# Optimization experiments

Measured on AMD Instinct MI355X. Metric: run time of the kernel, lower is better.

## Reference

```python
import jax, jax.numpy as jnp
import numpy as np

DIM, N_HEAD, N_KV, HEAD_DIM = 2048, 16, 4, 128
ROPE_BASE = 10000.0
ROPE_FACTOR = 1.0  # YaRN with factor=1 == plain RoPE


def setup_inputs() -> dict:
    key = jax.random.key(0)
    k1, k2, k3, k4 = jax.random.split(key, 4)
    b, s = 4, 2048
    sc = 1.0 / np.sqrt(DIM)
    return {
        "x": jax.random.normal(k1, (b, s, DIM), dtype=jnp.float32),
        "Wq": jax.random.normal(k2, (DIM, DIM), dtype=jnp.float32) * sc,
        "Wkv": jax.random.normal(k3, (2 * N_KV * HEAD_DIM, DIM), dtype=jnp.float32) * sc,
        "Wo": jax.random.normal(k4, (DIM, DIM), dtype=jnp.float32) * sc,
    }


def _rope_cos_sin(seqlen, start_pos=0):
    inv_freq = 1.0 / (ROPE_BASE ** (jnp.arange(0, HEAD_DIM, 2, dtype=jnp.float32) / HEAD_DIM))
    pos = (jnp.arange(seqlen, dtype=jnp.float32) + start_pos) / ROPE_FACTOR
    ang = pos[:, None] * inv_freq  # (s, hd/2)
    cos = jnp.concatenate([jnp.cos(ang), jnp.cos(ang)], axis=-1)  # (s, hd)
    sin = jnp.concatenate([jnp.sin(ang), jnp.sin(ang)], axis=-1)
    return cos[None, :, None, :], sin[None, :, None, :]  # (1, s, 1, hd)


def _rotate_half(t):
    h = HEAD_DIM // 2
    return jnp.concatenate([-t[..., h:], t[..., :h]], axis=-1)


def reference(x, Wq, Wkv, Wo):
    b, s, dim = x.shape
    G = N_HEAD // N_KV  # query heads per kv head
    q = (x @ Wq.T).reshape(b, s, N_HEAD, HEAD_DIM)                 # (b,s,H,hd)
    kv = (x @ Wkv.T).reshape(b, s, 2, N_KV, HEAD_DIM)
    k, v = kv[:, :, 0], kv[:, :, 1]                                # (b,s,KV,hd)
    cos, sin = _rope_cos_sin(s)
    q = q * cos + _rotate_half(q) * sin
    k = k * cos + _rotate_half(k) * sin
    # grouped attention: head h attends kv head h // G (matches repeat_interleave)
    qg = q.transpose(0, 2, 1, 3).reshape(b, N_KV, G, s, HEAD_DIM)  # (b,KV,G,s,hd)
    kt = k.transpose(0, 2, 1, 3)                                   # (b,KV,s,hd)
    vt = v.transpose(0, 2, 1, 3)
    scale = 1.0 / jnp.sqrt(jnp.asarray(HEAD_DIM, dtype=x.dtype))
    scores = jnp.einsum('bkgqd,bkpd->bkgqp', qg, kt) * scale       # (b,KV,G,s,s)
    causal = jnp.tril(jnp.ones((s, s), dtype=bool))
    scores = jnp.where(causal, scores, jnp.asarray(-jnp.inf, dtype=scores.dtype))
    probs = jax.nn.softmax(scores, axis=-1)
    out = jnp.einsum('bkgqp,bkpd->bkgqd', probs, vt)               # (b,KV,G,s,hd)
    out = out.reshape(b, N_HEAD, s, HEAD_DIM).transpose(0, 2, 1, 3).reshape(b, s, dim)
    return out @ Wo.T
```

## Files before the change

### kernel.cpp

```cpp
#include <hip/hip_runtime.h>
#include <hip/hip_bf16.h>

typedef __hip_bfloat16 bf16;
typedef __attribute__((ext_vector_type(4))) float f32x4;
typedef __attribute__((ext_vector_type(16))) float f32x16;
typedef __attribute__((ext_vector_type(8))) short short8;
typedef __attribute__((ext_vector_type(4))) unsigned u32x4;

#define NHEAD 16
#define NKV 4
#define HD 128
#define BATCH 4
#define SEQ 2048
#define DIMM 2048
#define NROWS (BATCH*SEQ)
#define QKVN (DIMM + 2*NKV*HD)

__device__ inline void gload_lds16(const bf16* g, bf16* l) {
  __builtin_amdgcn_global_load_lds(
      (const __attribute__((address_space(1))) unsigned int*)g,
      (__attribute__((address_space(3))) unsigned int*)l, 16, 0, 0);
}

__device__ inline unsigned cvtpk(float a, float b) {
  unsigned r;
  asm("v_cvt_pk_bf16_f32 %0, %1, %2" : "=v"(r) : "v"(a), "v"(b));
  return r;
}
__device__ inline void pswap(unsigned& x, unsigned& y) {
  asm volatile("v_permlane32_swap_b32 %0, %1" : "+v"(x), "+v"(y));
}
__device__ inline float bf2f(short s) {
  return __uint_as_float(((unsigned)(unsigned short)s) << 16);
}
__device__ inline short f2bfbits(float f) {
  bf16 h = __float2bfloat16(f);
  return *reinterpret_cast<short*>(&h);
}

#define CVTN0 ((size_t)NROWS * DIMM)
#define CVTN1 ((size_t)DIMM * DIMM)
#define CVTN2 ((size_t)2 * NKV * HD * DIMM)
#define CVTN3 ((size_t)DIMM * DIMM)
__global__ void cvt_all(const float* __restrict__ x, const float* __restrict__ wq,
                        const float* __restrict__ wkv, const float* __restrict__ wo,
                        bf16* __restrict__ xb, bf16* __restrict__ wqb,
                        bf16* __restrict__ wkvb, bf16* __restrict__ wob) {
  const size_t total = CVTN0 + CVTN1 + CVTN2 + CVTN3;
  for (size_t i = ((size_t)blockIdx.x * blockDim.x + threadIdx.x) * 4; i < total;
       i += (size_t)gridDim.x * blockDim.x * 4) {
    const float* s;
    bf16* d;
    size_t off;
    if (i < CVTN0) { s = x; d = xb; off = i; }
    else if (i < CVTN0 + CVTN1) { s = wq; d = wqb; off = i - CVTN0; }
    else if (i < CVTN0 + CVTN1 + CVTN2) { s = wkv; d = wkvb; off = i - CVTN0 - CVTN1; }
    else { s = wo; d = wob; off = i - CVTN0 - CVTN1 - CVTN2; }
    const float4 v = *reinterpret_cast<const float4*>(s + off);
    alignas(8) bf16 t[4] = {__float2bfloat16(v.x), __float2bfloat16(v.y),
                            __float2bfloat16(v.z), __float2bfloat16(v.w)};
    *reinterpret_cast<uint2*>(d + off) = *reinterpret_cast<const uint2*>(t);
  }
}

__device__ inline void store_c(float* p, float v) { *p = v; }
__device__ inline void store_c(bf16* p, float v) { *p = __float2bfloat16(v); }

template <typename OutT>
__global__ __launch_bounds__(512, 2) void gemm256(
    const bf16* __restrict__ A, const bf16* __restrict__ B0,
    const bf16* __restrict__ B1, OutT* __restrict__ C,
    int N, int K, int Nsplit, int MI8) {
  __shared__ __align__(16) short As[2][2][256 * 32];
  __shared__ __align__(16) short Bs[2][2][256 * 32];
  const int tid = threadIdx.x;
  const int w = tid >> 6, l = tid & 63;
  const int bid = blockIdx.x;
  const int xcd = bid & 7, q = bid >> 3;
  const int mi = q % MI8, j = q / MI8;
  const int m0 = (xcd * MI8 + mi) * 256, n0 = j * 256;
  const bf16* Ap = A + (size_t)m0 * K;
  const bf16* Bp = (n0 < Nsplit) ? (B0 + (size_t)n0 * K)
                                 : (B1 + (size_t)(n0 - Nsplit) * K);
  const int wr = w >> 2, wc = w & 3;
  const int lr = l & 15, lc = l >> 4;
  const int swz = lc ^ (((lr >> 3) & 1) << 1);

  f32x4 acc[8][4] = {};
  const int KT = K >> 6;

  auto stage = [&](int kt, int kh, int buf) {
#pragma unroll
    for (int jj = 0; jj < 2; ++jj) {
      const int cbase = jj * 512 + w * 64;
      const int ch = cbase + l;
      const int row = ch >> 2, c = ch & 3;
      const int sc = c ^ (((row >> 3) & 1) << 1);
      const int gcol = kt * 64 + kh * 32 + sc * 8;
      gload_lds16(Ap + (size_t)row * K + gcol, (bf16*)&As[buf][kh][cbase * 8]);
      gload_lds16(Bp + (size_t)row * K + gcol, (bf16*)&Bs[buf][kh][cbase * 8]);
    }
  };

  stage(0, 0, 0);
  stage(0, 1, 0);
  stage(1, 0, 1);

  for (int kt = 0; kt < KT; ++kt) {
    const int cur = kt & 1;
#pragma unroll
    for (int kh = 0; kh < 2; ++kh) {
      if (kt < KT - 1) {
        asm volatile("s_waitcnt vmcnt(8)" ::: "memory");
      } else if (kh == 0) {
        asm volatile("s_waitcnt vmcnt(4)" ::: "memory");
      } else {
        asm volatile("s_waitcnt vmcnt(0)" ::: "memory");
      }
      __builtin_amdgcn_s_barrier();
      __builtin_amdgcn_sched_barrier(0);

      short8 a[8], b[4];
      const short* Ab = &As[cur][kh][0];
      const short* Bb = &Bs[cur][kh][0];
#pragma unroll
      for (int mr = 0; mr < 8; ++mr)
        a[mr] = *(const short8*)&Ab[(wr * 128 + mr * 16 + lr) * 32 + swz * 8];
#pragma unroll
      for (int nr = 0; nr < 4; ++nr)
        b[nr] = *(const short8*)&Bb[(wc * 64 + nr * 16 + lr) * 32 + swz * 8];

      {
        const int g = 2 * kt + kh + 3;
        const int st = g >> 1;
        if (st < KT) stage(st, g & 1, st & 1);
      }

      __builtin_amdgcn_s_setprio(1);
#pragma unroll
      for (int mr = 0; mr < 8; ++mr)
#pragma unroll
        for (int nr = 0; nr < 4; ++nr)
          acc[mr][nr] = __builtin_amdgcn_mfma_f32_16x16x32_bf16(
              a[mr], b[nr], acc[mr][nr], 0, 0, 0);
      __builtin_amdgcn_s_setprio(0);
    }
  }

  const int cr4 = (l >> 4) * 4;
#pragma unroll
  for (int mr = 0; mr < 8; ++mr)
#pragma unroll
    for (int nr = 0; nr < 4; ++nr)
#pragma unroll
      for (int r = 0; r < 4; ++r) {
        const int row = m0 + wr * 128 + mr * 16 + cr4 + r;
        const int col = n0 + wc * 64 + nr * 16 + lr;
        store_c(&C[(size_t)row * N + col], acc[mr][nr][r]);
      }
}

__global__ void rope_kernel(bf16* __restrict__ qkv) {
  const int idx = blockIdx.x * blockDim.x + threadIdx.x;
  const int dc = idx & 7;
  const int slot = (idx >> 3) % 20;
  const int row = idx / (8 * 20);
  const int col = (slot < 16) ? slot * 128 : DIMM + (slot - 16) * 128;
  const size_t base = (size_t)row * QKVN + col;
  const int pos = row & (SEQ - 1);
  const float psc = (slot < 16) ? 0.12751879895f : 1.0f;
  short8 lo = *(const short8*)(qkv + base + dc * 8);
  short8 hi = *(const short8*)(qkv + base + 64 + dc * 8);
  short8 olo, ohi;
#pragma unroll
  for (int j = 0; j < 8; ++j) {
    const int d = dc * 8 + j;
    const float inv = exp2f((float)d * (-2.0f / 128.0f) * 13.287712379549449f);
    float sn, cs;
    __sincosf((float)pos * inv, &sn, &cs);
    const float flo = bf2f(lo[j]), fhi = bf2f(hi[j]);
    olo[j] = f2bfbits((flo * cs - fhi * sn) * psc);
    ohi[j] = f2bfbits((fhi * cs + flo * sn) * psc);
  }
  *(short8*)(qkv + base + dc * 8) = olo;
  *(short8*)(qkv + base + 64 + dc * 8) = ohi;
}

__global__ __launch_bounds__(256) void vtrans_kernel(const bf16* __restrict__ qkv,
                                                     bf16* __restrict__ vtg) {
  __shared__ short T[64 * 72];
  const int si = blockIdx.x * 64;
  const int di = blockIdx.y * 64;
  const int b = blockIdx.z >> 2, kvh = blockIdx.z & 3;
  const int t = threadIdx.x;
  const int r = t >> 2, c2 = (t & 3) * 2;
  const bf16* src =
      qkv + (size_t)(b * SEQ + si + r) * QKVN + DIMM + NKV * HD + kvh * 128 + di;
#pragma unroll
  for (int i = 0; i < 2; ++i)
    *(short8*)&T[r * 72 + (c2 + i) * 8] = *(const short8*)(src + (c2 + i) * 8);
  __syncthreads();
#pragma unroll
  for (int i = 0; i < 2; ++i) {
    short8 v;
    const int s8 = (c2 + i) * 8;
#pragma unroll
    for (int j = 0; j < 8; ++j) v[j] = T[(s8 + j) * 72 + r];
    *(short8*)(vtg + (size_t)(kvh * 128 + di + r) * NROWS + b * SEQ + si + s8) = v;
  }
}

__global__ __launch_bounds__(512, 2) void attn_kernel(
    const bf16* __restrict__ qkv, const bf16* __restrict__ vtg,
    bf16* __restrict__ aout) {
  __shared__ __align__(16) short KsL[2][64 * 128];
  __shared__ __align__(16) short VtL[2][128 * 64];
  const int tid = threadIdx.x, w = tid >> 6, l = tid & 63;
  const int lq = l & 31, hi = l >> 5;
  const int id = blockIdx.x;
  const int half = id >> 8, rr = id & 255;
  const int bh = (rr >> 3) + half * 32;
  const int j = rr & 7;
  const int qb = half ? j : 7 - j;
  const int b = bh >> 4, h = bh & 15, kvh = h >> 2;
  const int qw0 = qb * 256 + w * 32;
  const int qg = qw0 + lq;

  short8 qf[8];
  {
    const bf16* qptr = qkv + (size_t)(b * SEQ + qg) * QKVN + h * 128 + hi * 8;
#pragma unroll
    for (int s = 0; s < 8; ++s) qf[s] = *(const short8*)(qptr + s * 16);
  }

  f32x16 o[4] = {};
  float m = -1e30f, lsum = 0.f;
  const int ntiles = qb * 4 + 4;

  const bf16* Kgb = qkv + (size_t)(b * SEQ) * QKVN + DIMM + kvh * 128;
  const bf16* Vgb = vtg + (size_t)kvh * 128 * NROWS + b * SEQ;

  auto stage = [&](int kt, int buf) {
#pragma unroll
    for (int rd = 0; rd < 2; ++rd) {
      const int cb = (w * 2 + rd) * 64;
      {
        const int lc = cb + l, k = lc >> 4, c = lc & 15;
        gload_lds16(Kgb + (size_t)(kt * 64 + k) * QKVN + ((c ^ (k & 7)) * 8),
                    (bf16*)&KsL[buf][cb * 8]);
      }
      {
        const int lc = cb + l, d = lc >> 3, c = lc & 7;
        gload_lds16(Vgb + (size_t)d * NROWS + kt * 64 + ((c ^ (d & 7)) * 8),
                    (bf16*)&VtL[buf][cb * 8]);
      }
    }
  };

  stage(0, 0);
  asm volatile("s_waitcnt vmcnt(0)" ::: "memory");
  __builtin_amdgcn_s_barrier();
  __builtin_amdgcn_sched_barrier(0);

  for (int kt = 0; kt < ntiles; ++kt) {
    const int cur = kt & 1;
    if (kt + 1 < ntiles) stage(kt + 1, cur ^ 1);

    if (kt * 64 <= qw0 + 31) {
      f32x16 st[2];
#pragma unroll
      for (int ks = 0; ks < 2; ++ks) {
        const short* kb = &KsL[cur][(ks * 32 + lq) * 128];
        const int r7 = lq & 7;
        f32x16 acc = {};
#pragma unroll
        for (int s = 0; s < 8; ++s) {
          const short8 kf = *(const short8*)&kb[((2 * s + hi) ^ r7) * 8];
          acc = __builtin_amdgcn_mfma_f32_32x32x16_bf16(kf, qf[s], acc, 0, 0, 0);
        }
        st[ks] = acc;
      }
      if (kt * 64 + 63 > qw0) {
#pragma unroll
        for (int ks = 0; ks < 2; ++ks)
#pragma unroll
          for (int r = 0; r < 16; ++r) {
            const int kg = kt * 64 + ks * 32 + (r & 3) + 8 * (r >> 2) + 4 * hi;
            if (kg > qg) st[ks][r] = -1e30f;
          }
      }
      float t[16];
#pragma unroll
      for (int r = 0; r < 16; ++r) t[r] = fmaxf(st[0][r], st[1][r]);
#pragma unroll
      for (int d2 = 8; d2 > 0; d2 >>= 1)
#pragma unroll
        for (int r = 0; r < 8; ++r)
          if (r < d2) t[r] = fmaxf(t[r], t[r + d2]);
      float pm = fmaxf(t[0], __shfl_xor(t[0], 32));
      if (!__all(pm <= m + 11.0f)) {
        const float mnew = fmaxf(m, pm);
        const float fsc = __builtin_amdgcn_exp2f(m - mnew);
        m = mnew;
        lsum *= fsc;
#pragma unroll
        for (int r = 0; r < 16; ++r) {
          const float fq = __shfl(fsc, (r & 3) + 8 * (r >> 2) + 4 * hi);
#pragma unroll
          for (int db = 0; db < 4; ++db) o[db][r] *= fq;
        }
      }
      short8 pa[4];
#pragma unroll
      for (int ks = 0; ks < 2; ++ks) {
        float p[16];
        float s0 = 0.f, s1 = 0.f, s2 = 0.f, s3 = 0.f;
#pragma unroll
        for (int r = 0; r < 16; r += 4) {
          p[r] = __builtin_amdgcn_exp2f(st[ks][r] - m);         s0 += p[r];
          p[r + 1] = __builtin_amdgcn_exp2f(st[ks][r + 1] - m); s1 += p[r + 1];
          p[r + 2] = __builtin_amdgcn_exp2f(st[ks][r + 2] - m); s2 += p[r + 2];
          p[r + 3] = __builtin_amdgcn_exp2f(st[ks][r + 3] - m); s3 += p[r + 3];
        }
        lsum += (s0 + s1) + (s2 + s3);
#pragma unroll
        for (int hf = 0; hf < 2; ++hf) {
          unsigned x0 = cvtpk(p[hf * 8 + 0], p[hf * 8 + 1]);
          unsigned y0 = cvtpk(p[hf * 8 + 4], p[hf * 8 + 5]);
          unsigned x1 = cvtpk(p[hf * 8 + 2], p[hf * 8 + 3]);
          unsigned y1 = cvtpk(p[hf * 8 + 6], p[hf * 8 + 7]);
          pswap(x0, y0);
          pswap(x1, y1);
          union { u32x4 u; short8 s; } pk;
          pk.u = u32x4{x0, x1, y0, y1};
          pa[ks * 2 + hf] = pk.s;
        }
      }
#pragma unroll
      for (int s = 0; s < 4; ++s) {
        const int cc = ((2 * s + hi) ^ (lq & 7)) * 8;
#pragma unroll
        for (int db = 0; db < 4; ++db) {
          const short8 vb = *(const short8*)&VtL[cur][(db * 32 + lq) * 64 + cc];
          o[db] = __builtin_amdgcn_mfma_f32_32x32x16_bf16(pa[s], vb, o[db], 0, 0, 0);
        }
      }
    }

    asm volatile("s_waitcnt vmcnt(0)" ::: "memory");
    __builtin_amdgcn_s_barrier();
    __builtin_amdgcn_sched_barrier(0);
  }

  const float lf = lsum + __shfl_xor(lsum, 32);
#pragma unroll
  for (int r = 0; r < 16; ++r) {
    const int qr = (r & 3) + 8 * (r >> 2) + 4 * hi;
    const float linv = 1.0f / __shfl(lf, qr);
    bf16* op = aout + (size_t)(b * SEQ + qw0 + qr) * DIMM + h * 128 + lq;
#pragma unroll
    for (int db = 0; db < 4; ++db)
      op[db * 32] = __float2bfloat16(o[db][r] * linv);
  }
}

extern "C" void kernel_launch(void* const* d_in, const int* in_sizes, int n_in,
                              void* d_out, int out_size, void* d_ws, size_t ws_size,
                              hipStream_t stream) {
  const float* x = (const float*)d_in[0];
  const float* Wq = (const float*)d_in[1];
  const float* Wkv = (const float*)d_in[2];
  const float* Wo = (const float*)d_in[3];
  float* out = (float*)d_out;

  bf16* xb = (bf16*)d_ws;
  bf16* Wqb = xb + (size_t)NROWS * DIMM;
  bf16* Wkvb = Wqb + (size_t)DIMM * DIMM;
  bf16* Wob = Wkvb + (size_t)2 * NKV * HD * DIMM;
  bf16* attn = Wob + (size_t)DIMM * DIMM;
  bf16* qkv = (bf16*)d_out;
  bf16* vtg = (bf16*)d_out + (size_t)NROWS * QKVN;

  cvt_all<<<2048, 256, 0, stream>>>(x, Wq, Wkv, Wo, xb, Wqb, Wkvb, Wob);

  gemm256<bf16><<<dim3((NROWS / 256) * (QKVN / 256)), 512, 0, stream>>>(
      xb, Wqb, Wkvb, qkv, QKVN, DIMM, DIMM, (NROWS / 256) / 8);

  rope_kernel<<<(NROWS * 20 * 8) / 256, 256, 0, stream>>>(qkv);

  vtrans_kernel<<<dim3(SEQ / 64, 2, 16), 256, 0, stream>>>(qkv, vtg);

  attn_kernel<<<dim3(512), 512, 0, stream>>>(qkv, vtg, attn);

  gemm256<float><<<dim3((NROWS / 256) * (DIMM / 256)), 512, 0, stream>>>(
      attn, Wob, Wob, out, DIMM, DIMM, DIMM, (NROWS / 256) / 8);
}
```

Measured before the change: 305.7 us.

## Split GEMM inner step into two halves interleaving global-to-LDS staging with MFMAs

```diff
diff --git a/kernel.cpp b/kernel.cpp
--- a/kernel.cpp
+++ b/kernel.cpp
@@ -89,27 +89,28 @@
   f32x4 acc[8][4] = {};
   const int KT = K >> 6;
 
-  auto stage = [&](int kt, int kh, int buf) {
-#pragma unroll
-    for (int jj = 0; jj < 2; ++jj) {
-      const int cbase = jj * 512 + w * 64;
-      const int ch = cbase + l;
-      const int row = ch >> 2, c = ch & 3;
-      const int sc = c ^ (((row >> 3) & 1) << 1);
-      const int gcol = kt * 64 + kh * 32 + sc * 8;
-      gload_lds16(Ap + (size_t)row * K + gcol, (bf16*)&As[buf][kh][cbase * 8]);
-      gload_lds16(Bp + (size_t)row * K + gcol, (bf16*)&Bs[buf][kh][cbase * 8]);
-    }
+  auto stage_half = [&](int g, int jj) {
+    const int st = g >> 1;
+    if (st >= KT) return;
+    const int stkh = g & 1, buf = st & 1;
+    const int cbase = jj * 512 + w * 64;
+    const int ch = cbase + l;
+    const int row = ch >> 2, c = ch & 3;
+    const int sc = c ^ (((row >> 3) & 1) << 1);
+    const int gcol = st * 64 + stkh * 32 + sc * 8;
+    gload_lds16(Ap + (size_t)row * K + gcol, (bf16*)&As[buf][stkh][cbase * 8]);
+    gload_lds16(Bp + (size_t)row * K + gcol, (bf16*)&Bs[buf][stkh][cbase * 8]);
   };
 
-  stage(0, 0, 0);
-  stage(0, 1, 0);
-  stage(1, 0, 1);
+  stage_half(0, 0); stage_half(0, 1);
+  stage_half(1, 0); stage_half(1, 1);
+  stage_half(2, 0); stage_half(2, 1);
 
   for (int kt = 0; kt < KT; ++kt) {
     const int cur = kt & 1;
 #pragma unroll
     for (int kh = 0; kh < 2; ++kh) {
+      const int g = 2 * kt + kh;
       if (kt < KT - 1) {
         asm volatile("s_waitcnt vmcnt(8)" ::: "memory");
       } else if (kh == 0) {
@@ -120,29 +121,44 @@
       __builtin_amdgcn_s_barrier();
       __builtin_amdgcn_sched_barrier(0);
 
-      short8 a[8], b[4];
       const short* Ab = &As[cur][kh][0];
       const short* Bb = &Bs[cur][kh][0];
-#pragma unroll
-      for (int mr = 0; mr < 8; ++mr)
-        a[mr] = *(const short8*)&Ab[(wr * 128 + mr * 16 + lr) * 32 + swz * 8];
+
+      short8 a0[4], b[4];
+#pragma unroll
+      for (int mr = 0; mr < 4; ++mr)
+        a0[mr] = *(const short8*)&Ab[(wr * 128 + mr * 16 + lr) * 32 + swz * 8];
 #pragma unroll
       for (int nr = 0; nr < 4; ++nr)
         b[nr] = *(const short8*)&Bb[(wc * 64 + nr * 16 + lr) * 32 + swz * 8];
-
-      {
-        const int g = 2 * kt + kh + 3;
-        const int st = g >> 1;
-        if (st < KT) stage(st, g & 1, st & 1);
-      }
-
+      stage_half(g + 3, 0);
+      __builtin_amdgcn_s_barrier();
+      asm volatile("s_waitcnt lgkmcnt(0)" ::: "memory");
+      __builtin_amdgcn_sched_barrier(0);
       __builtin_amdgcn_s_setprio(1);
 #pragma unroll
-      for (int mr = 0; mr < 8; ++mr)
+      for (int mr = 0; mr < 4; ++mr)
 #pragma unroll
         for (int nr = 0; nr < 4; ++nr)
           acc[mr][nr] = __builtin_amdgcn_mfma_f32_16x16x32_bf16(
-              a[mr], b[nr], acc[mr][nr], 0, 0, 0);
+              a0[mr], b[nr], acc[mr][nr], 0, 0, 0);
+      __builtin_amdgcn_s_setprio(0);
+
+      short8 a1[4];
+#pragma unroll
+      for (int mr = 0; mr < 4; ++mr)
+        a1[mr] = *(const short8*)&Ab[(wr * 128 + (mr + 4) * 16 + lr) * 32 + swz * 8];
+      stage_half(g + 3, 1);
+      __builtin_amdgcn_s_barrier();
+      asm volatile("s_waitcnt lgkmcnt(0)" ::: "memory");
+      __builtin_amdgcn_sched_barrier(0);
+      __builtin_amdgcn_s_setprio(1);
+#pragma unroll
+      for (int mr = 0; mr < 4; ++mr)
+#pragma unroll
+        for (int nr = 0; nr < 4; ++nr)
+          acc[mr + 4][nr] = __builtin_amdgcn_mfma_f32_16x16x32_bf16(
+              a1[mr], b[nr], acc[mr + 4][nr], 0, 0, 0);
       __builtin_amdgcn_s_setprio(0);
     }
   }
```

Measured after the change: 319.3 us. 4.4% more time.
